# Kernel optimization log

Measured on AMD Instinct MI355X. Metric: run time of the kernel, lower is better.

Reference implementation:

```python
import jax, jax.numpy as jnp
import numpy as np

N_NODES = 50000
N_EDGES = 1600000
IN_SIZE = 128
NUM_HEADS = 4
OUT_SIZE = 32


def setup_inputs() -> dict:
    key = jax.random.key(0)
    k1, k2, k3, k4 = jax.random.split(key, 4)
    feat = jax.random.normal(k1, (N_NODES, IN_SIZE), dtype=jnp.float32)
    src = jax.random.randint(k2, (N_EDGES,), 0, N_NODES)
    dst = jnp.sort(jax.random.randint(k3, (N_EDGES,), 0, N_NODES))
    # fc weight of DGL DotGatConv: Linear(in_size, num_heads*out_size, bias=False)
    W = jax.random.normal(k4, (IN_SIZE, NUM_HEADS * OUT_SIZE), dtype=jnp.float32) * 0.05
    return {"feat": feat, "src": src, "dst": dst, "W": W}


def reference(feat, src, dst, W):
    N = feat.shape[0]
    H, D = NUM_HEADS, OUT_SIZE
    # project: [N, H, D]
    h = (feat @ W).reshape(N, H, D)
    h_src = h[src]            # [E, H, D] gather
    h_dst = h[dst]            # [E, H, D] gather
    # per-edge dot-product attention score, scaled by sqrt(out_size)
    e = jnp.sum(h_src * h_dst, axis=-1) / jnp.sqrt(jnp.asarray(D, h.dtype))  # [E, H]
    # edge softmax over incoming edges of each destination node
    m = jax.ops.segment_max(e, dst, num_segments=N)        # [N, H]
    ex = jnp.exp(e - m[dst])                               # [E, H]
    s = jax.ops.segment_sum(ex, dst, num_segments=N)       # [N, H]
    alpha = ex / s[dst]                                    # [E, H]
    # weighted aggregation of source features: sum_e alpha_e * h_src_e -> dst
    out = jax.ops.segment_sum(alpha[:, :, None] * h_src, dst, num_segments=N)  # [N, H, D]
    return out
```

## Files before the change

### kernel.cpp

```cpp
#include <hip/hip_runtime.h>
#include <math.h>

#define N_NODES 50000
#define N_EDGES 1600000
#define IN_SIZE 128
#define HD 128
#define NUM_HEADS 4
#define OUT_SIZE 32
#define STRIPS (N_NODES / 16)
#define PROJ_BLOCKS ((STRIPS + 3) / 4)
#define OFF_BLOCKS ((N_NODES + 1 + 255) / 256)

#define SCALE2 0.25503486f

typedef _Float16 half8 __attribute__((ext_vector_type(8)));
typedef _Float16 half2v __attribute__((ext_vector_type(2)));
typedef __attribute__((ext_vector_type(4))) float floatx4;

static __device__ __forceinline__ half2v pk_f16(float a, float b) {
#if __has_builtin(__builtin_amdgcn_cvt_pkrtz)
    auto r = __builtin_amdgcn_cvt_pkrtz(a, b);
    union { decltype(r) i; half2v o; } u;
    u.i = r;
    return u.o;
#else
    half2v r; r.x = (_Float16)a; r.y = (_Float16)b; return r;
#endif
}

static __device__ __forceinline__ float dot2(half2v a, half2v b, float c) {
#if __has_builtin(__builtin_amdgcn_fdot2)
    return __builtin_amdgcn_fdot2(a, b, c, false);
#else
    return fmaf((float)a.x, (float)b.x, fmaf((float)a.y, (float)b.y, c));
#endif
}

__global__ __launch_bounds__(256) void k_pre(const float* __restrict__ feat,
                                             const float* __restrict__ W,
                                             const int* __restrict__ dst,
                                             _Float16* __restrict__ hb,
                                             int* __restrict__ off) {
    if (blockIdx.x >= PROJ_BLOCKS) {
        int i = (blockIdx.x - PROJ_BLOCKS) * 256 + threadIdx.x;
        if (i <= N_NODES) {
            int lo = 0, hi = N_EDGES;
            while (lo < hi) {
                int mid = (lo + hi) >> 1;
                if (dst[mid] < i) lo = mid + 1; else hi = mid;
            }
            off[i] = lo;
        }
        return;
    }

    __shared__ _Float16 WF[32 * 64 * 8];

    int tid = threadIdx.x;
#pragma unroll
    for (int i = 0; i < 8; i++) {
        int entry = tid + 256 * i;
        int fl = entry & 63;
        int fi = entry >> 6;
        int t = fi >> 2, kb = fi & 3;
        int fq = fl >> 4, fl15 = fl & 15;
        int c = t * 16 + fl15;
        int k0 = kb * 32 + fq * 8;
        union { half8 v; half2v h[4]; } bu;
#pragma unroll
        for (int j = 0; j < 4; j++) {
            float lo = W[(size_t)(k0 + 2 * j) * HD + c];
            float hi = W[(size_t)(k0 + 2 * j + 1) * HD + c];
            bu.h[j] = pk_f16(lo, hi);
        }
        *(half8*)&WF[entry * 8] = bu.v;
    }
    __syncthreads();

    int wave = tid >> 6, lane = tid & 63;
    int strip = blockIdx.x * 4 + wave;
    if (strip >= STRIPS) return;
    int quad = lane >> 4, l15 = lane & 15;
    int row = strip * 16 + l15;

    const float* abp = feat + (size_t)row * IN_SIZE + quad * 8;
    float4 a[8];
#pragma unroll
    for (int kb = 0; kb < 4; kb++) {
        a[2 * kb]     = *(const float4*)(abp + kb * 32);
        a[2 * kb + 1] = *(const float4*)(abp + kb * 32 + 4);
    }

    floatx4 acc[8];
#pragma unroll
    for (int t = 0; t < 8; t++) acc[t] = (floatx4)(0.f);

#pragma unroll
    for (int kb = 0; kb < 4; kb++) {
        float4 x = a[2 * kb], y = a[2 * kb + 1];
        union { half8 v; half2v h[4]; } af;
        af.h[0] = pk_f16(x.x, x.y);
        af.h[1] = pk_f16(x.z, x.w);
        af.h[2] = pk_f16(y.x, y.y);
        af.h[3] = pk_f16(y.z, y.w);
#pragma unroll
        for (int t = 0; t < 8; t++) {
            half8 bf = *(const half8*)&WF[(size_t)((t * 4 + kb) * 64 + lane) * 8];
            acc[t] = __builtin_amdgcn_mfma_f32_16x16x32_f16(af.v, bf, acc[t], 0, 0, 0);
        }
    }

#pragma unroll
    for (int t = 0; t < 8; t++) {
#pragma unroll
        for (int r = 0; r < 4; r++) {
            int R = strip * 16 + quad * 4 + r;
            hb[(size_t)R * HD + t * 16 + l15] = (_Float16)acc[t][r];
        }
    }
}

__global__ __launch_bounds__(256) void k_edge(const _Float16* __restrict__ hb,
                                              const int* __restrict__ src,
                                              const int* __restrict__ off,
                                              float* __restrict__ out) {
    int n = (blockIdx.x * 256 + threadIdx.x) >> 6;
    int lane = threadIdx.x & 63;
    if (n >= N_NODES) return;
    int e0 = off[n], e1 = off[n + 1];

    int g = lane >> 4;
    int p = lane & 15;

    const uint4* h4 = (const uint4*)hb;
    union U { uint4 v; half2v h[4]; };

    U hdv; hdv.v = h4[(size_t)n * 16 + p];
    half2v hdc[4];
    half2v sc2 = pk_f16(SCALE2, SCALE2);
#pragma unroll
    for (int d = 0; d < 4; d++) hdc[d] = hdv.h[d] * sc2;

    float s = 0.f;
    half2v acc2[4];
#pragma unroll
    for (int d = 0; d < 4; d++) acc2[d] = (half2v)(_Float16)0.f;

    int iters = (e1 - e0 + 3) >> 2;
    int ntrip = (iters + 3) >> 2;

    int ecur = e0 + g;
    U buf[4]; bool ba[4];
#pragma unroll
    for (int j = 0; j < 4; j++) {
        int ej = ecur + 4 * j;
        ba[j] = (ej < e1);
        int sj = ba[j] ? src[ej] : n;
        buf[j].v = h4[(size_t)sj * 16 + p];
    }

    for (int it = 0; it < ntrip; it++) {
#pragma unroll
        for (int j = 0; j < 4; j++) {
            int ep = ecur + 16;
            bool ap = (ep < e1);
            int sp = ap ? src[ep] : n;
            U nb; nb.v = h4[(size_t)sp * 16 + p];

            float p0 = dot2(buf[j].h[0], hdc[0], 0.f);
            float p1 = dot2(buf[j].h[1], hdc[1], 0.f);
            p0 = dot2(buf[j].h[2], hdc[2], p0);
            p1 = dot2(buf[j].h[3], hdc[3], p1);
            float pd = p0 + p1;
            pd += __shfl_xor(pd, 1);
            pd += __shfl_xor(pd, 2);
            float w = ba[j] ? __builtin_amdgcn_exp2f(pd) : 0.f;
            s += w;
            half2v wh = pk_f16(w, w);
#pragma unroll
            for (int d = 0; d < 4; d++) acc2[d] += buf[j].h[d] * wh;

            buf[j] = nb; ba[j] = ap;
            ecur += 4;
        }
    }

    union B { half2v h; int i; };
#pragma unroll
    for (int d = 16; d <= 32; d <<= 1) {
        s += __shfl_xor(s, d);
#pragma unroll
        for (int j = 0; j < 4; j++) {
            B b; b.h = acc2[j];
            b.i = __shfl_xor(b.i, d);
            acc2[j] += b.h;
        }
    }

    if (g == 0) {
        float inv = (s > 0.f) ? 1.f / s : 0.f;
        float4 o0, o1;
        o0.x = (float)acc2[0].x * inv; o0.y = (float)acc2[0].y * inv;
        o0.z = (float)acc2[1].x * inv; o0.w = (float)acc2[1].y * inv;
        o1.x = (float)acc2[2].x * inv; o1.y = (float)acc2[2].y * inv;
        o1.z = (float)acc2[3].x * inv; o1.w = (float)acc2[3].y * inv;
        float4* op = (float4*)(out + (size_t)n * HD + 8 * p);
        op[0] = o0;
        op[1] = o1;
    }
}

extern "C" void kernel_launch(void* const* d_in, const int* in_sizes, int n_in,
                              void* d_out, int out_size, void* d_ws, size_t ws_size,
                              hipStream_t stream) {
    const float* feat = (const float*)d_in[0];
    const int*   src  = (const int*)d_in[1];
    const int*   dst  = (const int*)d_in[2];
    const float* W    = (const float*)d_in[3];
    float* out = (float*)d_out;

    char* ws = (char*)d_ws;
    _Float16* hb = (_Float16*)ws;
    int* off = (int*)(ws + (size_t)N_NODES * HD * 2);

    k_pre<<<PROJ_BLOCKS + OFF_BLOCKS, 256, 0, stream>>>(feat, W, dst, hb, off);
    k_edge<<<(N_NODES + 3) / 4, 256, 0, stream>>>(hb, src, off, out);
}
```

Measured before the change: 149.1 us.

## Preload source indices per 64-edge chunk and deepen gather prefetch to 8

Each wave now loads up to 64 source indices with one coalesced load per chunk, distributes them with lane shuffles, and prefetches the next chunk's indices ahead of time. This removes the dependent per-edge src load that came before each feature gather. The gather pipeline is also doubled from 4 to 8 in-flight row loads per 16-lane group using two register buffers. The cost is more VGPRs, which may lower occupancy, plus extra shuffle instructions per edge.

```diff
diff --git a/kernel.cpp b/kernel.cpp
--- a/kernel.cpp
+++ b/kernel.cpp
@@ -128,12 +128,15 @@
     int lane = threadIdx.x & 63;
     if (n >= N_NODES) return;
     int e0 = off[n], e1 = off[n + 1];
+    int deg = e1 - e0;
 
     int g = lane >> 4;
     int p = lane & 15;
 
     const uint4* h4 = (const uint4*)hb;
     union U { uint4 v; half2v h[4]; };
+
+    int sl_cur = (e0 + lane < e1) ? src[e0 + lane] : n;
 
     U hdv; hdv.v = h4[(size_t)n * 16 + p];
     half2v hdc[4];
@@ -146,43 +149,92 @@
 #pragma unroll
     for (int d = 0; d < 4; d++) acc2[d] = (half2v)(_Float16)0.f;
 
-    int iters = (e1 - e0 + 3) >> 2;
-    int ntrip = (iters + 3) >> 2;
-
-    int ecur = e0 + g;
-    U buf[4]; bool ba[4];
-#pragma unroll
-    for (int j = 0; j < 4; j++) {
-        int ej = ecur + 4 * j;
-        ba[j] = (ej < e1);
-        int sj = ba[j] ? src[ej] : n;
-        buf[j].v = h4[(size_t)sj * 16 + p];
-    }
-
-    for (int it = 0; it < ntrip; it++) {
-#pragma unroll
-        for (int j = 0; j < 4; j++) {
-            int ep = ecur + 16;
-            bool ap = (ep < e1);
-            int sp = ap ? src[ep] : n;
-            U nb; nb.v = h4[(size_t)sp * 16 + p];
-
-            float p0 = dot2(buf[j].h[0], hdc[0], 0.f);
-            float p1 = dot2(buf[j].h[1], hdc[1], 0.f);
-            p0 = dot2(buf[j].h[2], hdc[2], p0);
-            p1 = dot2(buf[j].h[3], hdc[3], p1);
-            float pd = p0 + p1;
-            pd += __shfl_xor(pd, 1);
-            pd += __shfl_xor(pd, 2);
-            float w = ba[j] ? __builtin_amdgcn_exp2f(pd) : 0.f;
-            s += w;
-            half2v wh = pk_f16(w, w);
-#pragma unroll
-            for (int d = 0; d < 4; d++) acc2[d] += buf[j].h[d] * wh;
-
-            buf[j] = nb; ba[j] = ap;
-            ecur += 4;
-        }
+    int nchunks = (deg + 63) >> 6;
+    int eb = e0;
+
+    for (int c = 0; c < nchunks; c++) {
+        int sl_next = n;
+        if (c + 1 < nchunks) {
+            int en = eb + 64 + lane;
+            sl_next = (en < e1) ? src[en] : n;
+        }
+
+        int cdeg = e1 - eb;
+        if (cdeg > 64) cdeg = 64;
+        int nsteps = (cdeg + 3) >> 2;
+        int ntrips = (nsteps + 7) >> 3;
+
+        U bufA[4], bufB[4];
+        bool baA[4], baB[4];
+#pragma unroll
+        for (int j = 0; j < 4; j++) {
+            int ei = 4 * j + g;
+            baA[j] = (ei < cdeg);
+            int sj = __shfl(sl_cur, ei);
+            sj = baA[j] ? sj : n;
+            bufA[j].v = h4[(size_t)sj * 16 + p];
+        }
+#pragma unroll
+        for (int j = 0; j < 4; j++) {
+            int ei = 4 * (j + 4) + g;
+            baB[j] = (ei < cdeg);
+            int sj = __shfl(sl_cur, ei & 63);
+            sj = baB[j] ? sj : n;
+            bufB[j].v = h4[(size_t)sj * 16 + p];
+        }
+
+        for (int it = 0; it < ntrips; it++) {
+            int tau0 = it * 8;
+#pragma unroll
+            for (int j = 0; j < 4; j++) {
+                int ei = 4 * (tau0 + j + 8) + g;
+                bool ap = (ei < cdeg);
+                int sp = __shfl(sl_cur, ei & 63);
+                sp = ap ? sp : n;
+                U nb; nb.v = h4[(size_t)sp * 16 + p];
+
+                float p0 = dot2(bufA[j].h[0], hdc[0], 0.f);
+                float p1 = dot2(bufA[j].h[1], hdc[1], 0.f);
+                p0 = dot2(bufA[j].h[2], hdc[2], p0);
+                p1 = dot2(bufA[j].h[3], hdc[3], p1);
+                float pd = p0 + p1;
+                pd += __shfl_xor(pd, 1);
+                pd += __shfl_xor(pd, 2);
+                float w = baA[j] ? __builtin_amdgcn_exp2f(pd) : 0.f;
+                s += w;
+                half2v wh = pk_f16(w, w);
+#pragma unroll
+                for (int d = 0; d < 4; d++) acc2[d] += bufA[j].h[d] * wh;
+
+                bufA[j] = nb; baA[j] = ap;
+            }
+#pragma unroll
+            for (int j = 0; j < 4; j++) {
+                int ei = 4 * (tau0 + j + 12) + g;
+                bool ap = (ei < cdeg);
+                int sp = __shfl(sl_cur, ei & 63);
+                sp = ap ? sp : n;
+                U nb; nb.v = h4[(size_t)sp * 16 + p];
+
+                float p0 = dot2(bufB[j].h[0], hdc[0], 0.f);
+                float p1 = dot2(bufB[j].h[1], hdc[1], 0.f);
+                p0 = dot2(bufB[j].h[2], hdc[2], p0);
+                p1 = dot2(bufB[j].h[3], hdc[3], p1);
+                float pd = p0 + p1;
+                pd += __shfl_xor(pd, 1);
+                pd += __shfl_xor(pd, 2);
+                float w = baB[j] ? __builtin_amdgcn_exp2f(pd) : 0.f;
+                s += w;
+                half2v wh = pk_f16(w, w);
+#pragma unroll
+                for (int d = 0; d < 4; d++) acc2[d] += bufB[j].h[d] * wh;
+
+                bufB[j] = nb; baB[j] = ap;
+            }
+        }
+
+        eb += 64;
+        sl_cur = sl_next;
     }
 
     union B { half2v h; int i; };
```

Result: faster. 145.6 us (-2.4%).
